# Kernel tuning notes

Hardware: AMD Instinct MI355X
Metric: run time of the kernel (lower is better)

Reference implementation:

```python
import jax, jax.numpy as jnp
import numpy as np

N_NODES = 100000
N_EDGES = 3200000
IN_FEAT = 256   # dim * decoder_heads = 128 * 2
HEADS = 2
N_CLASSES = 8
CURV = 1.0
NEG_SLOPE = 0.2
EPS = 1e-15


def setup_inputs() -> dict:
    key = jax.random.key(0)
    ks = jax.random.split(key, 7)
    x = jax.random.normal(ks[0], (N_NODES, IN_FEAT), dtype=jnp.float32) * 0.1
    edge_index = jax.random.randint(ks[1], (2, N_EDGES), 0, N_NODES, dtype=jnp.int64)
    W = jax.random.normal(ks[2], (IN_FEAT, HEADS * N_CLASSES), dtype=jnp.float32) * (1.0 / np.sqrt(IN_FEAT))
    attn_l = jax.random.normal(ks[3], (HEADS, N_CLASSES), dtype=jnp.float32) * 0.1
    attn_r = jax.random.normal(ks[4], (HEADS, N_CLASSES), dtype=jnp.float32) * 0.1
    bias = jnp.zeros((HEADS, N_CLASSES), dtype=jnp.float32)
    W_res = jax.random.normal(ks[5], (IN_FEAT, HEADS * N_CLASSES), dtype=jnp.float32) * (1.0 / np.sqrt(IN_FEAT))
    return {"x": x, "edge_index": edge_index, "W": W, "attn_l": attn_l,
            "attn_r": attn_r, "bias": bias, "W_res": W_res}


def _artanh(z):
    z = jnp.clip(z, -1.0 + 1e-7, 1.0 - 1e-7)
    return 0.5 * (jnp.log1p(z) - jnp.log1p(-z))


def _logmap0_poincare(x, c):
    # PoincareBall.logmap0; proj_tan0 is identity for the Poincare ball.
    sqrt_c = jnp.sqrt(c)
    norm = jnp.maximum(jnp.linalg.norm(x, axis=-1, keepdims=True), EPS)
    scale = _artanh(sqrt_c * norm) / (sqrt_c * norm)
    return scale * x


def reference(x, edge_index, W, attn_l, attn_r, bias, W_res):
    N = x.shape[0]
    # hyperbolic -> tangent space at origin
    h = _logmap0_poincare(x, CURV)                               # [N, F]
    # GATConv (DGL-style), dropout disabled (eval)
    feat = (h @ W).reshape(N, HEADS, N_CLASSES)                  # [N, H, C]
    el = jnp.einsum('nhc,hc->nh', feat, attn_l)                  # [N, H]
    er = jnp.einsum('nhc,hc->nh', feat, attn_r)                  # [N, H]
    src, dst = edge_index[0], edge_index[1]
    e = el[src] + er[dst]                                        # [E, H]
    e = jnp.where(e >= 0, e, NEG_SLOPE * e)                      # leaky_relu
    # edge softmax over incoming edges of each destination node
    m = jax.ops.segment_max(e, dst, num_segments=N)              # [N, H]
    m = jnp.where(jnp.isfinite(m), m, 0.0)
    e_exp = jnp.exp(e - m[dst])                                  # [E, H]
    denom = jax.ops.segment_sum(e_exp, dst, num_segments=N)      # [N, H]
    alpha = e_exp / jnp.maximum(denom[dst], EPS)                 # [E, H]
    # aggregate messages
    msg = alpha[:, :, None] * feat[src]                          # [E, H, C]
    rst = jax.ops.segment_sum(msg, dst, num_segments=N)          # [N, H, C]
    # residual + bias
    rst = rst + (h @ W_res).reshape(N, HEADS, N_CLASSES) + bias
    # Decoder.decode: probs.mean(dim=1) over heads
    return rst.mean(axis=1)                                      # [N, C]
```

## Files before the change

kernel.cpp:

```cpp
#include <hip/hip_runtime.h>
#include <math.h>

#define N_NODES 100000
#define N_EDGES 3200000
#define IN_FEAT 256
#define HEADS 2
#define NC 8
#define FH 16
#define NEG_SLOPE 0.2f
#define EPSF 1e-15f

#define BSH 6
#define BUCK_W 64
#define DLM 63
#define NBUCK ((N_NODES + BUCK_W - 1) / BUCK_W)
#define B1 256
#define EPB (N_EDGES / B1)

#define SORT_CAP 2560
#define RCAP (SORT_CAP / 256)
#define TPD 4

typedef float f32x4 __attribute__((ext_vector_type(4)));
typedef short bf16x8 __attribute__((ext_vector_type(8)));

__device__ __forceinline__ unsigned short f2bf(float f) {
    unsigned u = __float_as_uint(f);
    u += 0x7FFFu + ((u >> 16) & 1u);
    return (unsigned short)(u >> 16);
}
__device__ __forceinline__ float bflo(unsigned u) { return __uint_as_float(u << 16); }
__device__ __forceinline__ float bfhi(unsigned u) { return __uint_as_float(u & 0xFFFF0000u); }

__device__ __forceinline__ int chunk_of_block(int bid) {
    return (bid & 7) * (B1 / 8) + (bid >> 3);
}

__global__ __launch_bounds__(256) void k_node(
        const float* __restrict__ x, const float* __restrict__ W,
        const float* __restrict__ Wres, const float* __restrict__ attn_l,
        const float* __restrict__ attn_r, const int* __restrict__ ei,
        unsigned short* __restrict__ featb, float* __restrict__ res,
        float* __restrict__ el, float* __restrict__ er,
        int* __restrict__ hist_g) {
    __shared__ int h[NBUCK];
    int t = threadIdx.x;
    bool do_count = (blockIdx.x < B1);
    if (do_count) {
        for (int i = t; i < NBUCK; i += 256) h[i] = 0;
    }

    int wid = (blockIdx.x * 256 + t) >> 6;
    int n0 = wid * 16;
    if (n0 < N_NODES) {
        int l   = t & 63;
        int col = l & 15;
        int g   = l >> 4;

        bf16x8 bw[8], bq[8];
        #pragma unroll
        for (int kk = 0; kk < 8; kk++) {
            #pragma unroll
            for (int j = 0; j < 8; j++) {
                int k = kk * 32 + g * 8 + j;
                bw[kk][j] = (short)f2bf(W[k * FH + col]);
                bq[kk][j] = (short)f2bf(Wres[k * FH + col]);
            }
        }

        const float* xr = x + (size_t)(n0 + col) * IN_FEAT;
        f32x4 acc0 = {0.f, 0.f, 0.f, 0.f};
        f32x4 acc1 = {0.f, 0.f, 0.f, 0.f};
        float ss = 0.f;
        #pragma unroll
        for (int kk = 0; kk < 8; kk++) {
            float4 v0 = *(const float4*)(xr + kk * 32 + g * 8);
            float4 v1 = *(const float4*)(xr + kk * 32 + g * 8 + 4);
            ss += v0.x * v0.x + v0.y * v0.y + v0.z * v0.z + v0.w * v0.w
                + v1.x * v1.x + v1.y * v1.y + v1.z * v1.z + v1.w * v1.w;
            bf16x8 a;
            a[0] = (short)f2bf(v0.x); a[1] = (short)f2bf(v0.y);
            a[2] = (short)f2bf(v0.z); a[3] = (short)f2bf(v0.w);
            a[4] = (short)f2bf(v1.x); a[5] = (short)f2bf(v1.y);
            a[6] = (short)f2bf(v1.z); a[7] = (short)f2bf(v1.w);
            acc0 = __builtin_amdgcn_mfma_f32_16x16x32_bf16(a, bw[kk], acc0, 0, 0, 0);
            acc1 = __builtin_amdgcn_mfma_f32_16x16x32_bf16(a, bq[kk], acc1, 0, 0, 0);
        }

        ss += __shfl_xor(ss, 16);
        ss += __shfl_xor(ss, 32);
        float norm = fmaxf(sqrtf(ss), EPSF);
        float z = fminf(norm, 1.f - 1e-7f);
        float at = 0.5f * (log1pf(z) - log1pf(-z));
        float scale = at / norm;

        float alc = attn_l[col], arc = attn_r[col];

        #pragma unroll
        for (int i = 0; i < 4; i++) {
            int ri = g * 4 + i;
            float s_i = __shfl(scale, ri);
            int nr = n0 + ri;
            float f_i = acc0[i] * s_i;
            float q_i = acc1[i] * s_i;
            featb[(size_t)nr * FH + col] = f2bf(f_i);
            res  [(size_t)nr * FH + col] = q_i;
            float pl = f_i * alc, pr = f_i * arc;
            float pl0 = (col < 8) ? pl : 0.f, pl1 = (col < 8) ? 0.f : pl;
            float pr0 = (col < 8) ? pr : 0.f, pr1 = (col < 8) ? 0.f : pr;
            #pragma unroll
            for (int m = 1; m < 16; m <<= 1) {
                pl0 += __shfl_xor(pl0, m); pl1 += __shfl_xor(pl1, m);
                pr0 += __shfl_xor(pr0, m); pr1 += __shfl_xor(pr1, m);
            }
            if (col == 0) {
                *(float2*)(el + nr * 2) = make_float2(pl0, pl1);
                *(float2*)(er + nr * 2) = make_float2(pr0, pr1);
            }
        }
    }

    if (do_count) {
        __syncthreads();
        int chunk = chunk_of_block(blockIdx.x);
        const int4* dp = (const int4*)(ei + N_EDGES + (size_t)chunk * EPB);
        for (int i = t; i < EPB / 4; i += 256) {
            int4 d = dp[i];
            atomicAdd(&h[d.x >> BSH], 1);
            atomicAdd(&h[d.y >> BSH], 1);
            atomicAdd(&h[d.z >> BSH], 1);
            atomicAdd(&h[d.w >> BSH], 1);
        }
        __syncthreads();
        int* outp = hist_g + (size_t)chunk * NBUCK;
        for (int i = t; i < NBUCK; i += 256) outp[i] = h[i];
    }
}

__global__ __launch_bounds__(64) void k_scan1(int* __restrict__ hist_g,
                                              int* __restrict__ btot) {
    __shared__ int sm[64];
    int bucket = blockIdx.x;
    int t = threadIdx.x;
    int carry = 0;
    for (int base = 0; base < B1; base += 64) {
        int blk = base + t;
        int v = hist_g[(size_t)blk * NBUCK + bucket];
        __syncthreads();
        sm[t] = v;
        __syncthreads();
        for (int off = 1; off < 64; off <<= 1) {
            int u = (t >= off) ? sm[t - off] : 0;
            __syncthreads();
            sm[t] += u;
            __syncthreads();
        }
        hist_g[(size_t)blk * NBUCK + bucket] = carry + sm[t] - v;
        carry += sm[63];
    }
    if (t == 0) btot[bucket] = carry;
}

__global__ __launch_bounds__(1024) void k_scan2(const int* __restrict__ btot,
                                                int* __restrict__ bstart) {
    __shared__ int sm[2048];
    int t = threadIdx.x;
    int i0 = t, i1 = t + 1024;
    int v0 = (i0 < NBUCK) ? btot[i0] : 0;
    int v1 = (i1 < NBUCK) ? btot[i1] : 0;
    sm[i0] = v0; sm[i1] = v1;
    __syncthreads();
    for (int d = 1; d < 2048; d <<= 1) {
        int a0 = (i0 >= d) ? sm[i0 - d] : 0;
        int a1 = (i1 >= d) ? sm[i1 - d] : 0;
        __syncthreads();
        sm[i0] += a0; sm[i1] += a1;
        __syncthreads();
    }
    if (i0 < NBUCK) bstart[i0] = sm[i0] - v0;
    if (i1 < NBUCK) bstart[i1] = sm[i1] - v1;
    if (t == 0) bstart[NBUCK] = sm[2047];
}

__global__ __launch_bounds__(1024) void k_scatter2(const int* __restrict__ ei,
                                                   const int* __restrict__ hist_g,
                                                   const int* __restrict__ bstart,
                                                   unsigned* __restrict__ packed) {
    __shared__ int cur[NBUCK];
    int chunk = chunk_of_block(blockIdx.x);
    const int* hrow = hist_g + (size_t)chunk * NBUCK;
    for (int i = threadIdx.x; i < NBUCK; i += 1024) cur[i] = bstart[i] + hrow[i];
    __syncthreads();
    size_t e0 = (size_t)chunk * EPB;
    const int4* sp = (const int4*)(ei + e0);
    const int4* dp = (const int4*)(ei + N_EDGES + e0);
    for (int i = threadIdx.x; i < EPB / 4; i += 1024) {
        int4 s = sp[i];
        int4 d = dp[i];
        int p0 = atomicAdd(&cur[d.x >> BSH], 1);
        int p1 = atomicAdd(&cur[d.y >> BSH], 1);
        int p2 = atomicAdd(&cur[d.z >> BSH], 1);
        int p3 = atomicAdd(&cur[d.w >> BSH], 1);
        packed[p0] = (unsigned)s.x | ((unsigned)(d.x & DLM) << 17);
        packed[p1] = (unsigned)s.y | ((unsigned)(d.y & DLM) << 17);
        packed[p2] = (unsigned)s.z | ((unsigned)(d.z & DLM) << 17);
        packed[p3] = (unsigned)s.w | ((unsigned)(d.w & DLM) << 17);
    }
}

__global__ __launch_bounds__(256) void k_aggsort(
        const unsigned* __restrict__ packed, const int* __restrict__ bstart,
        const float* __restrict__ el, const float* __restrict__ er,
        const unsigned short* __restrict__ featb, const float* __restrict__ res,
        const float* __restrict__ bias, float* __restrict__ out) {
    __shared__ int cnt[BUCK_W];
    __shared__ int off[BUCK_W];
    __shared__ unsigned srt[SORT_CAP];
    int b = blockIdx.x, t = threadIdx.x;
    int lo = bstart[b], hi = bstart[b + 1];

    if (t < BUCK_W) cnt[t] = 0;
    __syncthreads();

    unsigned pe[RCAP];
    int      tk[RCAP];
    #pragma unroll
    for (int i = 0; i < RCAP; i++) {
        int j = lo + i * 256 + t;
        if (j < hi) {
            unsigned p = packed[j];
            pe[i] = p;
            tk[i] = atomicAdd(&cnt[p >> 17], 1);
        } else {
            pe[i] = 0u; tk[i] = -1;
        }
    }
    __syncthreads();

    if (t < BUCK_W) off[t] = cnt[t];
    __syncthreads();
    #pragma unroll
    for (int d = 1; d < BUCK_W; d <<= 1) {
        int v = (t < BUCK_W && t >= d) ? off[t - d] : 0;
        __syncthreads();
        if (t < BUCK_W) off[t] += v;
        __syncthreads();
    }

    #pragma unroll
    for (int i = 0; i < RCAP; i++) {
        if (tk[i] >= 0) {
            int dl = (int)(pe[i] >> 17);
            srt[off[dl] - cnt[dl] + tk[i]] = pe[i] & 0x1FFFFu;
        }
    }
    __syncthreads();

    int dl = t >> 2, r = t & 3;
    int n = b * BUCK_W + dl;
    if (n >= N_NODES) return;
    int sBeg = off[dl] - cnt[dl];
    int sEnd = off[dl];
    float2 ern = *(const float2*)(er + n * 2);
    float den0 = 0.f, den1 = 0.f;
    float S[FH];
    #pragma unroll
    for (int k = 0; k < FH; k++) S[k] = 0.f;

    int j = sBeg + r;
    for (; j + 3 * TPD < sEnd; j += 4 * TPD) {
        int s0 = (int)srt[j];
        int s1 = (int)srt[j + TPD];
        int s2 = (int)srt[j + 2 * TPD];
        int s3 = (int)srt[j + 3 * TPD];
        float2 e0 = *(const float2*)(el + s0 * 2);
        float2 e1 = *(const float2*)(el + s1 * 2);
        float2 e2 = *(const float2*)(el + s2 * 2);
        float2 e3 = *(const float2*)(el + s3 * 2);
        const uint4* f0p = (const uint4*)(featb + (size_t)s0 * FH);
        const uint4* f1p = (const uint4*)(featb + (size_t)s1 * FH);
        const uint4* f2p = (const uint4*)(featb + (size_t)s2 * FH);
        const uint4* f3p = (const uint4*)(featb + (size_t)s3 * FH);
        uint4 u00 = f0p[0], u01 = f0p[1];
        uint4 u10 = f1p[0], u11 = f1p[1];
        uint4 u20 = f2p[0], u21 = f2p[1];
        uint4 u30 = f3p[0], u31 = f3p[1];
        float a0 = e0.x + ern.x, b0 = e0.y + ern.y;
        float a1 = e1.x + ern.x, b1 = e1.y + ern.y;
        float a2 = e2.x + ern.x, b2 = e2.y + ern.y;
        float a3 = e3.x + ern.x, b3 = e3.y + ern.y;
        a0 = a0 >= 0.f ? a0 : NEG_SLOPE * a0;  b0 = b0 >= 0.f ? b0 : NEG_SLOPE * b0;
        a1 = a1 >= 0.f ? a1 : NEG_SLOPE * a1;  b1 = b1 >= 0.f ? b1 : NEG_SLOPE * b1;
        a2 = a2 >= 0.f ? a2 : NEG_SLOPE * a2;  b2 = b2 >= 0.f ? b2 : NEG_SLOPE * b2;
        a3 = a3 >= 0.f ? a3 : NEG_SLOPE * a3;  b3 = b3 >= 0.f ? b3 : NEG_SLOPE * b3;
        float w00 = __expf(a0), w01 = __expf(b0);
        float w10 = __expf(a1), w11 = __expf(b1);
        float w20 = __expf(a2), w21 = __expf(b2);
        float w30 = __expf(a3), w31 = __expf(b3);
        den0 += w00 + w10 + w20 + w30;
        den1 += w01 + w11 + w21 + w31;
        S[0]  = fmaf(w00, bflo(u00.x), fmaf(w10, bflo(u10.x), fmaf(w20, bflo(u20.x), fmaf(w30, bflo(u30.x), S[0]))));
        S[1]  = fmaf(w00, bfhi(u00.x), fmaf(w10, bfhi(u10.x), fmaf(w20, bfhi(u20.x), fmaf(w30, bfhi(u30.x), S[1]))));
        S[2]  = fmaf(w00, bflo(u00.y), fmaf(w10, bflo(u10.y), fmaf(w20, bflo(u20.y), fmaf(w30, bflo(u30.y), S[2]))));
        S[3]  = fmaf(w00, bfhi(u00.y), fmaf(w10, bfhi(u10.y), fmaf(w20, bfhi(u20.y), fmaf(w30, bfhi(u30.y), S[3]))));
        S[4]  = fmaf(w00, bflo(u00.z), fmaf(w10, bflo(u10.z), fmaf(w20, bflo(u20.z), fmaf(w30, bflo(u30.z), S[4]))));
        S[5]  = fmaf(w00, bfhi(u00.z), fmaf(w10, bfhi(u10.z), fmaf(w20, bfhi(u20.z), fmaf(w30, bfhi(u30.z), S[5]))));
        S[6]  = fmaf(w00, bflo(u00.w), fmaf(w10, bflo(u10.w), fmaf(w20, bflo(u20.w), fmaf(w30, bflo(u30.w), S[6]))));
        S[7]  = fmaf(w00, bfhi(u00.w), fmaf(w10, bfhi(u10.w), fmaf(w20, bfhi(u20.w), fmaf(w30, bfhi(u30.w), S[7]))));
        S[8]  = fmaf(w01, bflo(u01.x), fmaf(w11, bflo(u11.x), fmaf(w21, bflo(u21.x), fmaf(w31, bflo(u31.x), S[8]))));
        S[9]  = fmaf(w01, bfhi(u01.x), fmaf(w11, bfhi(u11.x), fmaf(w21, bfhi(u21.x), fmaf(w31, bfhi(u31.x), S[9]))));
        S[10] = fmaf(w01, bflo(u01.y), fmaf(w11, bflo(u11.y), fmaf(w21, bflo(u21.y), fmaf(w31, bflo(u31.y), S[10]))));
        S[11] = fmaf(w01, bfhi(u01.y), fmaf(w11, bfhi(u11.y), fmaf(w21, bfhi(u21.y), fmaf(w31, bfhi(u31.y), S[11]))));
        S[12] = fmaf(w01, bflo(u01.z), fmaf(w11, bflo(u11.z), fmaf(w21, bflo(u21.z), fmaf(w31, bflo(u31.z), S[12]))));
        S[13] = fmaf(w01, bfhi(u01.z), fmaf(w11, bfhi(u11.z), fmaf(w21, bfhi(u21.z), fmaf(w31, bfhi(u31.z), S[13]))));
        S[14] = fmaf(w01, bflo(u01.w), fmaf(w11, bflo(u11.w), fmaf(w21, bflo(u21.w), fmaf(w31, bflo(u31.w), S[14]))));
        S[15] = fmaf(w01, bfhi(u01.w), fmaf(w11, bfhi(u11.w), fmaf(w21, bfhi(u21.w), fmaf(w31, bfhi(u31.w), S[15]))));
    }
    for (; j < sEnd; j += TPD) {
        int sa = (int)srt[j];
        float2 ea = *(const float2*)(el + sa * 2);
        float v0 = ea.x + ern.x, v1 = ea.y + ern.y;
        v0 = v0 >= 0.f ? v0 : NEG_SLOPE * v0;
        v1 = v1 >= 0.f ? v1 : NEG_SLOPE * v1;
        float w0 = __expf(v0), w1 = __expf(v1);
        den0 += w0; den1 += w1;
        const uint4* fp = (const uint4*)(featb + (size_t)sa * FH);
        uint4 u0 = fp[0], u1 = fp[1];
        S[0]  = fmaf(w0, bflo(u0.x), S[0]);  S[1]  = fmaf(w0, bfhi(u0.x), S[1]);
        S[2]  = fmaf(w0, bflo(u0.y), S[2]);  S[3]  = fmaf(w0, bfhi(u0.y), S[3]);
        S[4]  = fmaf(w0, bflo(u0.z), S[4]);  S[5]  = fmaf(w0, bfhi(u0.z), S[5]);
        S[6]  = fmaf(w0, bflo(u0.w), S[6]);  S[7]  = fmaf(w0, bfhi(u0.w), S[7]);
        S[8]  = fmaf(w1, bflo(u1.x), S[8]);  S[9]  = fmaf(w1, bfhi(u1.x), S[9]);
        S[10] = fmaf(w1, bflo(u1.y), S[10]); S[11] = fmaf(w1, bfhi(u1.y), S[11]);
        S[12] = fmaf(w1, bflo(u1.z), S[12]); S[13] = fmaf(w1, bfhi(u1.z), S[13]);
        S[14] = fmaf(w1, bflo(u1.w), S[14]); S[15] = fmaf(w1, bfhi(u1.w), S[15]);
    }

    #pragma unroll
    for (int k = 0; k < FH; k++) {
        S[k] += __shfl_xor(S[k], 1);
        S[k] += __shfl_xor(S[k], 2);
    }
    den0 += __shfl_xor(den0, 1); den0 += __shfl_xor(den0, 2);
    den1 += __shfl_xor(den1, 1); den1 += __shfl_xor(den1, 2);

    if (r == 0) {
        float inv0 = 1.f / fmaxf(den0, EPSF);
        float inv1 = 1.f / fmaxf(den1, EPSF);
        const float* rr = res + (size_t)n * FH;
        float4 r0a = *(const float4*)(rr + 0),  r0b = *(const float4*)(rr + 4);
        float4 r1a = *(const float4*)(rr + 8),  r1b = *(const float4*)(rr + 12);
        float4 oa, ob;
        oa.x = 0.5f * ((S[0] * inv0 + r0a.x + bias[0])  + (S[8]  * inv1 + r1a.x + bias[8]));
        oa.y = 0.5f * ((S[1] * inv0 + r0a.y + bias[1])  + (S[9]  * inv1 + r1a.y + bias[9]));
        oa.z = 0.5f * ((S[2] * inv0 + r0a.z + bias[2])  + (S[10] * inv1 + r1a.z + bias[10]));
        oa.w = 0.5f * ((S[3] * inv0 + r0a.w + bias[3])  + (S[11] * inv1 + r1a.w + bias[11]));
        ob.x = 0.5f * ((S[4] * inv0 + r0b.x + bias[4])  + (S[12] * inv1 + r1b.x + bias[12]));
        ob.y = 0.5f * ((S[5] * inv0 + r0b.y + bias[5])  + (S[13] * inv1 + r1b.y + bias[13]));
        ob.z = 0.5f * ((S[6] * inv0 + r0b.z + bias[6])  + (S[14] * inv1 + r1b.z + bias[14]));
        ob.w = 0.5f * ((S[7] * inv0 + r0b.w + bias[7])  + (S[15] * inv1 + r1b.w + bias[15]));
        *(float4*)(out + (size_t)n * NC + 0) = oa;
        *(float4*)(out + (size_t)n * NC + 4) = ob;
    }
}

extern "C" void kernel_launch(void* const* d_in, const int* in_sizes, int n_in,
                              void* d_out, int out_size, void* d_ws, size_t ws_size,
                              hipStream_t stream) {
    const float* x      = (const float*)d_in[0];
    const int*   ei     = (const int*)d_in[1];
    const float* W      = (const float*)d_in[2];
    const float* attn_l = (const float*)d_in[3];
    const float* attn_r = (const float*)d_in[4];
    const float* bias   = (const float*)d_in[5];
    const float* Wres   = (const float*)d_in[6];
    float* out = (float*)d_out;

    char* ws = (char*)d_ws;
    const size_t szFB   = (size_t)N_NODES * FH * sizeof(unsigned short);
    const size_t szNF   = (size_t)N_NODES * FH * sizeof(float);
    const size_t szNH   = (size_t)N_NODES * HEADS * sizeof(float);
    const size_t szHist = (((size_t)B1 * NBUCK * sizeof(int)) + 255) & ~(size_t)255;
    const size_t szBt   = 8192;
    size_t off = 0;
    unsigned short* featb = (unsigned short*)(ws + off); off += szFB;
    float*    res    = (float*)(ws + off); off += szNF;
    float*    el     = (float*)(ws + off); off += szNH;
    float*    er     = (float*)(ws + off); off += szNH;
    int*      hist_g = (int*)  (ws + off); off += szHist;
    int*      btot   = (int*)  (ws + off); off += szBt;
    int*      bstart = (int*)  (ws + off); off += szBt;
    unsigned* packed = (unsigned*)(ws + off); off += (size_t)N_EDGES * sizeof(unsigned);

    k_node<<<(N_NODES / 16 + 3) / 4, 256, 0, stream>>>(x, W, Wres, attn_l, attn_r,
                                                       ei, featb, res, el, er, hist_g);
    k_scan1<<<NBUCK, 64, 0, stream>>>(hist_g, btot);
    k_scan2<<<1, 1024, 0, stream>>>(btot, bstart);
    k_scatter2<<<B1, 1024, 0, stream>>>(ei, hist_g, bstart, packed);
    k_aggsort<<<NBUCK, 256, 0, stream>>>(packed, bstart, el, er, featb, res, bias, out);
}
```

Baseline: 109.9 us.

## Fuse bucket-total scan into scatter kernel and use intrinsic bf16 conversion

Removes the single-block k_scan2 launch. Every scatter block now redoes the 1563-entry prefix scan over bucket totals in shared memory, and block 0 also writes the global bucket starts that the aggregation kernel needs. This saves one kernel launch and its serial dependency, at the cost of redundant scan work in all 256 blocks. The hand-written float-to-bf16 rounding is also swapped for the HIP __float2bfloat16 intrinsic, which may lower to a hardware conversion.

```diff
diff --git a/kernel.cpp b/kernel.cpp
--- a/kernel.cpp
+++ b/kernel.cpp
@@ -1,4 +1,5 @@
 #include <hip/hip_runtime.h>
+#include <hip/hip_bf16.h>
 #include <math.h>
 
 #define N_NODES 100000
@@ -24,10 +25,10 @@
 typedef float f32x4 __attribute__((ext_vector_type(4)));
 typedef short bf16x8 __attribute__((ext_vector_type(8)));
 
-__device__ __forceinline__ unsigned short f2bf(float f) {
-    unsigned u = __float_as_uint(f);
-    u += 0x7FFFu + ((u >> 16) & 1u);
-    return (unsigned short)(u >> 16);
+__device__ __forceinline__ short f2bfs(float f) {
+    union { __hip_bfloat16 h; short s; } u;
+    u.h = __float2bfloat16(f);
+    return u.s;
 }
 __device__ __forceinline__ float bflo(unsigned u) { return __uint_as_float(u << 16); }
 __device__ __forceinline__ float bfhi(unsigned u) { return __uint_as_float(u & 0xFFFF0000u); }
@@ -63,8 +64,8 @@
             #pragma unroll
             for (int j = 0; j < 8; j++) {
                 int k = kk * 32 + g * 8 + j;
-                bw[kk][j] = (short)f2bf(W[k * FH + col]);
-                bq[kk][j] = (short)f2bf(Wres[k * FH + col]);
+                bw[kk][j] = f2bfs(W[k * FH + col]);
+                bq[kk][j] = f2bfs(Wres[k * FH + col]);
             }
         }
 
@@ -79,10 +80,10 @@
             ss += v0.x * v0.x + v0.y * v0.y + v0.z * v0.z + v0.w * v0.w
                 + v1.x * v1.x + v1.y * v1.y + v1.z * v1.z + v1.w * v1.w;
             bf16x8 a;
-            a[0] = (short)f2bf(v0.x); a[1] = (short)f2bf(v0.y);
-            a[2] = (short)f2bf(v0.z); a[3] = (short)f2bf(v0.w);
-            a[4] = (short)f2bf(v1.x); a[5] = (short)f2bf(v1.y);
-            a[6] = (short)f2bf(v1.z); a[7] = (short)f2bf(v1.w);
+            a[0] = f2bfs(v0.x); a[1] = f2bfs(v0.y);
+            a[2] = f2bfs(v0.z); a[3] = f2bfs(v0.w);
+            a[4] = f2bfs(v1.x); a[5] = f2bfs(v1.y);
+            a[6] = f2bfs(v1.z); a[7] = f2bfs(v1.w);
             acc0 = __builtin_amdgcn_mfma_f32_16x16x32_bf16(a, bw[kk], acc0, 0, 0, 0);
             acc1 = __builtin_amdgcn_mfma_f32_16x16x32_bf16(a, bq[kk], acc1, 0, 0, 0);
         }
@@ -103,7 +104,7 @@
             int nr = n0 + ri;
             float f_i = acc0[i] * s_i;
             float q_i = acc1[i] * s_i;
-            featb[(size_t)nr * FH + col] = f2bf(f_i);
+            featb[(size_t)nr * FH + col] = (unsigned short)f2bfs(f_i);
             res  [(size_t)nr * FH + col] = q_i;
             float pl = f_i * alc, pr = f_i * arc;
             float pl0 = (col < 8) ? pl : 0.f, pl1 = (col < 8) ? 0.f : pl;
@@ -161,10 +162,17 @@
     if (t == 0) btot[bucket] = carry;
 }
 
-__global__ __launch_bounds__(1024) void k_scan2(const int* __restrict__ btot,
-                                                int* __restrict__ bstart) {
+__global__ __launch_bounds__(1024) void k_scatter2(const int* __restrict__ ei,
+                                                   const int* __restrict__ hist_g,
+                                                   const int* __restrict__ btot,
+                                                   int* __restrict__ bstart_g,
+                                                   unsigned* __restrict__ packed) {
     __shared__ int sm[2048];
+    __shared__ int cur[NBUCK];
     int t = threadIdx.x;
+    int chunk = chunk_of_block(blockIdx.x);
+    const int* hrow = hist_g + (size_t)chunk * NBUCK;
+
     int i0 = t, i1 = t + 1024;
     int v0 = (i0 < NBUCK) ? btot[i0] : 0;
     int v1 = (i1 < NBUCK) ? btot[i1] : 0;
@@ -177,24 +185,19 @@
         sm[i0] += a0; sm[i1] += a1;
         __syncthreads();
     }
-    if (i0 < NBUCK) bstart[i0] = sm[i0] - v0;
-    if (i1 < NBUCK) bstart[i1] = sm[i1] - v1;
-    if (t == 0) bstart[NBUCK] = sm[2047];
-}
-
-__global__ __launch_bounds__(1024) void k_scatter2(const int* __restrict__ ei,
-                                                   const int* __restrict__ hist_g,
-                                                   const int* __restrict__ bstart,
-                                                   unsigned* __restrict__ packed) {
-    __shared__ int cur[NBUCK];
-    int chunk = chunk_of_block(blockIdx.x);
-    const int* hrow = hist_g + (size_t)chunk * NBUCK;
-    for (int i = threadIdx.x; i < NBUCK; i += 1024) cur[i] = bstart[i] + hrow[i];
-    __syncthreads();
+    if (i0 < NBUCK) cur[i0] = sm[i0] - v0 + hrow[i0];
+    if (i1 < NBUCK) cur[i1] = sm[i1] - v1 + hrow[i1];
+    if (blockIdx.x == 0) {
+        if (i0 < NBUCK) bstart_g[i0] = sm[i0] - v0;
+        if (i1 < NBUCK) bstart_g[i1] = sm[i1] - v1;
+        if (t == 0) bstart_g[NBUCK] = sm[2047];
+    }
+    __syncthreads();
+
     size_t e0 = (size_t)chunk * EPB;
     const int4* sp = (const int4*)(ei + e0);
     const int4* dp = (const int4*)(ei + N_EDGES + e0);
-    for (int i = threadIdx.x; i < EPB / 4; i += 1024) {
+    for (int i = t; i < EPB / 4; i += 1024) {
         int4 s = sp[i];
         int4 d = dp[i];
         int p0 = atomicAdd(&cur[d.x >> BSH], 1);
@@ -395,7 +398,6 @@
     k_node<<<(N_NODES / 16 + 3) / 4, 256, 0, stream>>>(x, W, Wres, attn_l, attn_r,
                                                        ei, featb, res, el, er, hist_g);
     k_scan1<<<NBUCK, 64, 0, stream>>>(hist_g, btot);
-    k_scan2<<<1, 1024, 0, stream>>>(btot, bstart);
-    k_scatter2<<<B1, 1024, 0, stream>>>(ei, hist_g, bstart, packed);
+    k_scatter2<<<B1, 1024, 0, stream>>>(ei, hist_g, btot, bstart, packed);
     k_aggsort<<<NBUCK, 256, 0, stream>>>(packed, bstart, el, er, featb, res, bias, out);
 }
```

Measured after the change: 108.4 us, median of 2. Within noise of the previous version (-1.4%).
